# Kernel tuning notes

Hardware: AMD Instinct MI355X
Metric: run time of the kernel (lower is better)

The kernel has to match this reference:

```python
import jax, jax.numpy as jnp
import numpy as np

HEAD_DIM = 128
NUM_Q_HEADS = 16
NUM_KV_HEADS = 8
EPS = 1e-6


def _rope_tables(seq_len, head_dim, base=10000.0):
    inv_freq = 1.0 / (base ** (np.arange(0, head_dim, 2, dtype=np.float32) / head_dim))
    t = np.arange(seq_len, dtype=np.float32)
    freqs = np.outer(t, inv_freq)                      # [S, hd/2]
    emb = np.concatenate([freqs, freqs], axis=-1)      # [S, hd]
    return jnp.asarray(np.cos(emb)), jnp.asarray(np.sin(emb))


def setup_inputs() -> dict:
    key = jax.random.key(0)
    k1, k2, k3 = jax.random.split(key, 3)
    B, S, D = 2, 2048, 2048
    qo_dim = NUM_Q_HEADS * HEAD_DIM
    kv_dim = NUM_KV_HEADS * HEAD_DIM
    x = jax.random.normal(k1, (B, S, D), dtype=jnp.float32)
    w_qkv = jax.random.normal(k2, (qo_dim + 2 * kv_dim, D), dtype=jnp.float32) * 0.02
    w_o = jax.random.normal(k3, (D, qo_dim), dtype=jnp.float32) * 0.02
    pos_cos, pos_sin = _rope_tables(S, HEAD_DIM)
    return {
        "x": x,
        "pos_cos": pos_cos,
        "pos_sin": pos_sin,
        "w_qkv": w_qkv,
        "w_o": w_o,
        "q_norm_w": jnp.ones((HEAD_DIM,), dtype=jnp.float32),
        "k_norm_w": jnp.ones((HEAD_DIM,), dtype=jnp.float32),
    }


def _rms_norm(h, w):
    # per-head RMSNorm over last dim (head_dim)
    var = jnp.mean(jnp.square(h), axis=-1, keepdims=True)
    return h * jax.lax.rsqrt(var + EPS) * w


def _rotate_half(h):
    h1, h2 = jnp.split(h, 2, axis=-1)
    return jnp.concatenate([-h2, h1], axis=-1)


def _apply_rope(h, cos, sin):
    # h: [B, S, H, hd]; cos/sin: [S, hd]
    c = cos[None, :, None, :]
    s = sin[None, :, None, :]
    return h * c + _rotate_half(h) * s


def reference(x, pos_cos, pos_sin, w_qkv, w_o, q_norm_w, k_norm_w):
    B, S, D = x.shape
    hd = HEAD_DIM
    qkv = jnp.einsum("bsd,ed->bse", x, w_qkv).reshape(B, S, -1, hd)
    q = qkv[:, :, :NUM_Q_HEADS]                                   # [B,S,Hq,hd]
    k = qkv[:, :, NUM_Q_HEADS:NUM_Q_HEADS + NUM_KV_HEADS]         # [B,S,Hk,hd]
    v = qkv[:, :, NUM_Q_HEADS + NUM_KV_HEADS:]                    # [B,S,Hk,hd]

    q = _apply_rope(_rms_norm(q, q_norm_w), pos_cos, pos_sin)
    k = _apply_rope(_rms_norm(k, k_norm_w), pos_cos, pos_sin)

    # GQA: expand kv heads to match query heads
    rep = NUM_Q_HEADS // NUM_KV_HEADS
    k = jnp.repeat(k, rep, axis=2)
    v = jnp.repeat(v, rep, axis=2)

    scale = 1.0 / jnp.sqrt(jnp.float32(hd))
    scores = jnp.einsum("bqhd,bkhd->bhqk", q, k) * scale          # [B,H,S,S]
    causal = jnp.tril(jnp.ones((S, S), dtype=bool))
    scores = jnp.where(causal[None, None], scores, jnp.finfo(scores.dtype).min)
    attn = jax.nn.softmax(scores, axis=-1)
    out = jnp.einsum("bhqk,bkhd->bqhd", attn, v)                  # [B,S,H,hd]
    out = out.reshape(B, S, NUM_Q_HEADS * hd)
    return jnp.einsum("bse,de->bsd", out, w_o)
```

## Files before the change

### kernel.cpp

```cpp
#include <hip/hip_runtime.h>
#include <hip/hip_bf16.h>
#include <stdint.h>

#define HD 128
#define NQH 16
#define NKVH 8
#define SEQ 2048
#define DMODEL 2048
#define BATCH 2

typedef __attribute__((ext_vector_type(8))) short bf16x8;
typedef __attribute__((ext_vector_type(4))) float f32x4;
typedef __attribute__((ext_vector_type(16))) float f32x16;

__device__ __forceinline__ ushort f2bf(float f){
  union { float f; uint32_t u; } v; v.f = f;
  uint32_t u = v.u;
  return (ushort)((u + 0x7FFFu + ((u >> 16) & 1u)) >> 16);
}
__device__ __forceinline__ float bf2f(ushort h){
  union { uint32_t u; float f; } v; v.u = ((uint32_t)h) << 16; return v.f;
}
__device__ __forceinline__ void gload16(const void* g, void* l){
  __builtin_amdgcn_global_load_lds((const __attribute__((address_space(1))) void*)g,
                                   (__attribute__((address_space(3))) void*)l, 16, 0, 0);
}
__device__ __forceinline__ unsigned int cvtpk(float lo, float hi){
  unsigned int r;
  asm("v_cvt_pk_bf16_f32 %0, %1, %2" : "=v"(r) : "v"(lo), "v"(hi));
  return r;
}

__global__ void cvtbf3(const float* __restrict__ x, const float* __restrict__ wqkv,
                       const float* __restrict__ wo,
                       ushort* __restrict__ xb, ushort* __restrict__ wqkvb,
                       ushort* __restrict__ wob){
  int bid = blockIdx.x;
  const float* in; ushort* out; int i;
  if (bid < 8192)       { in = x;    out = xb;    i = bid*256 + threadIdx.x; }
  else if (bid < 16384) { in = wqkv; out = wqkvb; i = (bid-8192)*256 + threadIdx.x; }
  else                  { in = wo;   out = wob;   i = (bid-16384)*256 + threadIdx.x; }
  float4 v = ((const float4*)in)[i];
  ushort4 o;
  o.x = f2bf(v.x); o.y = f2bf(v.y); o.z = f2bf(v.z); o.w = f2bf(v.w);
  ((ushort4*)out)[i] = o;
}

template<int OUTF32>
__global__ __launch_bounds__(256) void gemm_bt(const ushort* __restrict__ A,
                                               const ushort* __restrict__ B,
                                               void* __restrict__ C,
                                               int M, int N, int K){
  __shared__ __align__(16) ushort lA[128*64];
  __shared__ __align__(16) ushort lB[128*64];
  const int tid = threadIdx.x;
  const int l = tid & 63, w = tid >> 6;
  const int nwg = gridDim.x * gridDim.y;
  const int lin = blockIdx.y * gridDim.x + blockIdx.x;
  const int wg = (lin & 7) * (nwg >> 3) + (lin >> 3);
  const int m0 = (wg / gridDim.x) * 128, n0 = (wg % gridDim.x) * 128;
  const int wr = (w >> 1) * 64, wc = (w & 1) * 64;
  f32x4 acc[4][4];
  #pragma unroll
  for (int m=0;m<4;m++)
    #pragma unroll
    for (int n=0;n<4;n++) acc[m][n] = f32x4{0.f,0.f,0.f,0.f};

  const int srow = l >> 3;
  const int scol = ((l & 7) ^ srow) << 3;
  const ushort* gA = A + (size_t)(m0 + w*32 + srow) * K + scol;
  const ushort* gB = B + (size_t)(n0 + w*32 + srow) * K + scol;
  ushort* lAw = &lA[(w*32) * 64];
  ushort* lBw = &lB[(w*32) * 64];

  for (int kt = 0; kt < K; kt += 64){
    __syncthreads();
    #pragma unroll
    for (int j=0;j<4;j++){
      gload16(gA + kt + (size_t)(j*8)*K, lAw + j*8*64);
      gload16(gB + kt + (size_t)(j*8)*K, lBw + j*8*64);
    }
    __syncthreads();
    #pragma unroll
    for (int kk=0; kk<2; kk++){
      bf16x8 af[4], bb[4];
      #pragma unroll
      for (int m=0;m<4;m++){
        int row = wr + m*16 + (l & 15);
        int slot = (kk*4 + (l >> 4)) ^ (row & 7);
        af[m] = *(const bf16x8*)&lA[row*64 + slot*8];
      }
      #pragma unroll
      for (int n=0;n<4;n++){
        int row = wc + n*16 + (l & 15);
        int slot = (kk*4 + (l >> 4)) ^ (row & 7);
        bb[n] = *(const bf16x8*)&lB[row*64 + slot*8];
      }
      #pragma unroll
      for (int m=0;m<4;m++)
        #pragma unroll
        for (int n=0;n<4;n++)
          acc[m][n] = __builtin_amdgcn_mfma_f32_16x16x32_bf16(af[m], bb[n], acc[m][n], 0,0,0);
    }
  }
  #pragma unroll
  for (int m=0;m<4;m++)
    #pragma unroll
    for (int n=0;n<4;n++)
      #pragma unroll
      for (int r=0;r<4;r++){
        size_t row = (size_t)(m0 + wr + m*16 + (l>>4)*4 + r);
        size_t col = (size_t)(n0 + wc + n*16 + (l & 15));
        float v = acc[m][n][r];
        if (OUTF32) ((float*)C)[row*N + col] = v;
        else        ((ushort*)C)[row*N + col] = f2bf(v);
      }
}

__global__ __launch_bounds__(512, 1) void gemm256_bt(const ushort* __restrict__ A,
                                                     const ushort* __restrict__ B,
                                                     ushort* __restrict__ C,
                                                     int M, int N, int K){
  __shared__ __align__(16) ushort lA[2][256*64];
  __shared__ __align__(16) ushort lB[2][256*64];
  const int tid = threadIdx.x;
  const int l = tid & 63, w = tid >> 6;
  const int wm = w >> 2, wn = w & 3;
  const int nwg = gridDim.x * gridDim.y;
  const int lin = blockIdx.y * gridDim.x + blockIdx.x;
  const int wg = (lin & 7) * (nwg >> 3) + (lin >> 3);
  const int m0 = (wg / gridDim.x) * 256, n0 = (wg % gridDim.x) * 256;
  const int NT = K >> 6;

  const int srow = w*8 + (l >> 3);
  const int scol = ((l & 7) ^ (l >> 3)) << 3;

  const int la15 = l & 15;
  const int sl0 = (((l >> 4)    ) ^ (l & 7)) * 8;
  const int sl1 = ((4 + (l >> 4)) ^ (l & 7)) * 8;

  f32x4 acc[8][4];
  #pragma unroll
  for (int m=0;m<8;m++)
    #pragma unroll
    for (int n=0;n<4;n++) acc[m][n] = f32x4{0.f,0.f,0.f,0.f};

  auto stgA = [&](int t, int h){
    const int bi = t & 1;
    #pragma unroll
    for (int j=0;j<2;j++)
      gload16(A + (size_t)(m0 + h*128 + j*64 + srow)*K + t*64 + scol,
              &lA[bi][(h*128 + j*64 + w*8)*64]);
  };
  auto stgB = [&](int t, int h){
    const int bi = t & 1;
    #pragma unroll
    for (int j=0;j<2;j++)
      gload16(B + (size_t)(n0 + h*128 + j*64 + srow)*K + t*64 + scol,
              &lB[bi][(h*128 + j*64 + w*8)*64]);
  };

  stgA(0,0); stgA(0,1); stgB(0,0); stgB(0,1);
  stgA(1,0); stgB(1,0); stgB(1,1);
  asm volatile("s_waitcnt vmcnt(6)" ::: "memory");
  __builtin_amdgcn_s_barrier();

  for (int t2=0; t2<NT; t2+=2){
    #pragma unroll
    for (int tt=0; tt<2; tt++){
      const int t = t2 + tt;
      const ushort* pA = &lA[tt][(wm*128 + la15)*64];
      const ushort* pB = &lB[tt][(wn*64  + la15)*64];
      bf16x8 bfr0[4], bfr1[4];
      #pragma unroll
      for (int q=0; q<4; q++){
        bf16x8 af0[2], af1[2];
        #pragma unroll
        for (int mi2=0; mi2<2; mi2++){
          af0[mi2] = *(const bf16x8*)(pA + (q*32 + mi2*16)*64 + sl0);
          af1[mi2] = *(const bf16x8*)(pA + (q*32 + mi2*16)*64 + sl1);
        }
        if (q == 0){
          #pragma unroll
          for (int ni=0; ni<4; ni++){
            bfr0[ni] = *(const bf16x8*)(pB + ni*16*64 + sl0);
            bfr1[ni] = *(const bf16x8*)(pB + ni*16*64 + sl1);
          }
        }
        if (q == 0 && t+1 < NT) stgA(t+1, 1);
        if (q == 1 && t+2 < NT) stgB(t+2, 0);
        if (q == 2 && t+2 < NT) stgB(t+2, 1);
        __builtin_amdgcn_s_barrier();
        asm volatile("s_waitcnt lgkmcnt(0)" ::: "memory");
        if (q == 3 && t+2 < NT) stgA(t+2, 0);
        __builtin_amdgcn_s_setprio(1);
        #pragma unroll
        for (int mi2=0; mi2<2; mi2++)
          #pragma unroll
          for (int ni=0; ni<4; ni++)
            acc[q*2+mi2][ni] = __builtin_amdgcn_mfma_f32_16x16x32_bf16(
                af0[mi2], bfr0[ni], acc[q*2+mi2][ni], 0,0,0);
        #pragma unroll
        for (int mi2=0; mi2<2; mi2++)
          #pragma unroll
          for (int ni=0; ni<4; ni++)
            acc[q*2+mi2][ni] = __builtin_amdgcn_mfma_f32_16x16x32_bf16(
                af1[mi2], bfr1[ni], acc[q*2+mi2][ni], 0,0,0);
        __builtin_amdgcn_s_setprio(0);
        if (q == 3){
          if (t < NT-2) { asm volatile("s_waitcnt vmcnt(6)" ::: "memory"); }
          else          { asm volatile("s_waitcnt vmcnt(0)" ::: "memory"); }
        }
        __builtin_amdgcn_s_barrier();
      }
    }
  }

  #pragma unroll
  for (int mi=0; mi<8; mi++)
    #pragma unroll
    for (int ni=0; ni<4; ni++)
      #pragma unroll
      for (int r=0; r<4; r++){
        size_t row = (size_t)(m0 + wm*128 + mi*16 + (l>>4)*4 + r);
        size_t col = (size_t)(n0 + wn*64 + ni*16 + (l & 15));
        C[row*N + col] = f2bf(acc[mi][ni][r]);
      }
}

__global__ __launch_bounds__(256) void nr_vt(const ushort* __restrict__ qkv,
                                             const float* __restrict__ cosT,
                                             const float* __restrict__ sinT,
                                             const float* __restrict__ qw,
                                             const float* __restrict__ kw,
                                             ushort* __restrict__ Qo,
                                             ushort* __restrict__ Ko,
                                             ushort* __restrict__ vt){
  if (blockIdx.x < 24576){
    int gw = (blockIdx.x * 256 + threadIdx.x) >> 6;
    int l = threadIdx.x & 63;
    int head = gw % 24;
    int bs = gw / 24;
    int s = bs & (SEQ-1);
    int b = bs >> 11;
    ushort2 hv = *(const ushort2*)(qkv + (size_t)bs*(2*DMODEL) + head*HD + l*2);
    float h0 = bf2f(hv.x), h1 = bf2f(hv.y);
    float ss = h0*h0 + h1*h1;
    #pragma unroll
    for (int m=1; m<64; m<<=1) ss += __shfl_xor(ss, m);
    float rinv = rsqrtf(ss * (1.0f/128.0f) + 1e-6f);
    const float* wp = (head < NQH) ? qw : kw;
    float w0 = wp[l*2], w1 = wp[l*2+1];
    float n0 = h0 * rinv * w0, n1 = h1 * rinv * w1;
    float p0 = __shfl_xor(n0, 32), p1 = __shfl_xor(n1, 32);
    float r0 = (l < 32) ? -p0 : p0;
    float r1 = (l < 32) ? -p1 : p1;
    float c0 = cosT[s*HD + l*2], c1 = cosT[s*HD + l*2 + 1];
    float s0 = sinT[s*HD + l*2], s1 = sinT[s*HD + l*2 + 1];
    float sc = (head < NQH) ? 0.12751656062f : 1.0f;
    ushort2 o;
    o.x = f2bf((n0*c0 + r0*s0) * sc);
    o.y = f2bf((n1*c1 + r1*s1) * sc);
    if (head < NQH)
      *(ushort2*)(Qo + ((size_t)((b*NQH + head)*SEQ) + s)*HD + l*2) = o;
    else
      *(ushort2*)(Ko + ((size_t)((b*NKVH + (head-NQH))*SEQ) + s)*HD + l*2) = o;
  } else {
    __shared__ __align__(16) ushort t[64][136];
    int bid = blockIdx.x - 24576;
    int st = bid & 31, kh = (bid >> 5) & 7, b = bid >> 8;
    int s0 = st * 64;
    int tid = threadIdx.x;
    #pragma unroll
    for (int it=0; it<4; it++){
      int row = (tid >> 4) + it*16;
      int c = tid & 15;
      uint4 v = *(const uint4*)&qkv[((size_t)(b*SEQ + s0 + row))*(2*DMODEL) + (NQH+NKVH+kh)*HD + c*8];
      *(uint4*)&t[row][c*8] = v;
    }
    __syncthreads();
    #pragma unroll
    for (int it=0; it<4; it++){
      int g = it*256 + tid;
      int d = g >> 3, c = g & 7;
      ushort tmp[8] __attribute__((aligned(16)));
      #pragma unroll
      for (int j=0;j<8;j++) tmp[j] = t[c*8+j][d];
      *(uint4*)&vt[((size_t)((b*NKVH+kh)*HD + d))*SEQ + s0 + c*8] = *(uint4*)tmp;
    }
  }
}

__global__ __launch_bounds__(256, 2) void attn_fwd(const ushort* __restrict__ Q,
                                                   const ushort* __restrict__ Kb,
                                                   const ushort* __restrict__ Vt,
                                                   ushort* __restrict__ O){
  __shared__ __align__(16) ushort lK[2][64*128];
  __shared__ __align__(16) ushort lV[2][128*64];
  const int l = threadIdx.x & 63, w = threadIdx.x >> 6;
  const int wq = w >> 1, wkv = w & 1;
  const int hl = l >> 5, q32 = l & 31;
  const int lin = blockIdx.x;
  const int wg = (lin & 7) * 64 + (lin >> 3);
  const int e = wg & 15, head = (wg >> 4) & 15, b = wg >> 8;
  const int kh = head >> 1;

  const ushort* kg = Kb + (size_t)((b*NKVH + kh)*SEQ) * HD;
  const ushort* vg = Vt + (size_t)((b*NKVH + kh)*HD) * SEQ;

  auto STAGE = [&](int t, int bi){
    const int kv0 = t*64;
    #pragma unroll
    for (int j=0;j<4;j++){
      int krow = kv0 + w*16 + j*4 + (l>>4);
      gload16(kg + (size_t)krow*HD + (((l&15) ^ (krow&15))<<3),
              &lK[bi][(w*16 + j*4)*128]);
      int vrow = w*32 + j*8 + (l>>3);
      gload16(vg + (size_t)vrow*SEQ + kv0 + (((l&7) ^ (l>>3))<<3),
              &lV[bi][(w*32 + j*8)*64]);
    }
  };

  auto run_tile = [&](int qt){
    const int qb = qt*64 + wq*32;
    const ushort* qp = Q + ((size_t)((b*NQH + head)*SEQ) + qb + q32) * HD + hl*8;
    bf16x8 qf[8];
    #pragma unroll
    for (int ks=0; ks<8; ks++) qf[ks] = *(const bf16x8*)(qp + ks*16);

    float mrun = -1e30f, lrun = 0.f;
    f32x16 acc[4];
    #pragma unroll
    for (int dt=0;dt<4;dt++)
      #pragma unroll
      for (int r=0;r<16;r++) acc[dt][r] = 0.f;

    STAGE(0, 0);

    for (int t=0; t<=qt; t++){
      const int bi = t & 1;
      if (t < qt){
        STAGE(t+1, bi^1);
        asm volatile("s_waitcnt vmcnt(8)" ::: "memory");
      } else {
        asm volatile("s_waitcnt vmcnt(0)" ::: "memory");
      }
      __builtin_amdgcn_s_barrier();

      const bool skip = (t==qt) && (wq==0) && (wkv==1);
      if (!skip){
        f32x16 sa, sb;
        #pragma unroll
        for (int r=0;r<16;r++){ sa[r] = 0.f; sb[r] = 0.f; }
        const int rowT = wkv*32 + q32;
        __builtin_amdgcn_s_setprio(1);
        #pragma unroll
        for (int ks=0; ks<4; ks++){
          int slot0 = (ks*2 + hl) ^ (rowT & 15);
          int slot1 = ((ks+4)*2 + hl) ^ (rowT & 15);
          bf16x8 kf0 = *(const bf16x8*)&lK[bi][rowT*128 + slot0*8];
          bf16x8 kf1 = *(const bf16x8*)&lK[bi][rowT*128 + slot1*8];
          sa = __builtin_amdgcn_mfma_f32_32x32x16_bf16(kf0, qf[ks],   sa, 0,0,0);
          sb = __builtin_amdgcn_mfma_f32_32x32x16_bf16(kf1, qf[ks+4], sb, 0,0,0);
        }
        __builtin_amdgcn_s_setprio(0);
        f32x16 s = sa + sb;
        if (t==qt && wq==wkv){
          const int qg = qb + q32;
          #pragma unroll
          for (int r=0;r<16;r++){
            int kvg = t*64 + wkv*32 + (r&3) + 8*(r>>2) + 4*hl;
            s[r] = (kvg > qg) ? -1e30f : s[r];
          }
        }
        float m0 = fmaxf(fmaxf(s[0],s[1]),s[2]);
        float m1 = fmaxf(fmaxf(s[3],s[4]),s[5]);
        float m2 = fmaxf(fmaxf(s[6],s[7]),s[8]);
        float m3 = fmaxf(fmaxf(s[9],s[10]),s[11]);
        float m4 = fmaxf(fmaxf(s[12],s[13]),s[14]);
        float tmax = fmaxf(fmaxf(fmaxf(m0,m1),fmaxf(m2,m3)),fmaxf(m4,s[15]));
        tmax = fmaxf(tmax, __shfl_xor(tmax, 32));
        if (!__all(tmax <= mrun + 8.f)){
          float mnew = fmaxf(mrun, tmax);
          float corr = __builtin_amdgcn_exp2f(mrun - mnew);
          mrun = mnew; lrun *= corr;
          #pragma unroll
          for (int r=0;r<16;r++){
            int qr = (r&3) + 8*(r>>2) + 4*hl;
            float cr = __shfl(corr, qr);
            acc[0][r]*=cr; acc[1][r]*=cr; acc[2][r]*=cr; acc[3][r]*=cr;
          }
        }
        #pragma unroll
        for (int r=0;r<16;r++) s[r] = __builtin_amdgcn_exp2f(s[r] - mrun);
        float r0s = (s[0]+s[1])+(s[2]+s[3]);
        float r1s = (s[4]+s[5])+(s[6]+s[7]);
        float r2s = (s[8]+s[9])+(s[10]+s[11]);
        float r3s = (s[12]+s[13])+(s[14]+s[15]);
        float rs = (r0s+r1s)+(r2s+r3s);
        rs += __shfl_xor(rs, 32);
        lrun += rs;
        union PWU { unsigned int u[4]; bf16x8 v; };
        PWU pw0, pw1;
        {
          unsigned int A = cvtpk(s[0], s[1]);
          unsigned int B = cvtpk(s[2], s[3]);
          unsigned int C = cvtpk(s[4], s[5]);
          unsigned int D = cvtpk(s[6], s[7]);
          auto sw0 = __builtin_amdgcn_permlane32_swap(A, C, false, false);
          auto sw1 = __builtin_amdgcn_permlane32_swap(B, D, false, false);
          pw0.u[0]=sw0[0]; pw0.u[1]=sw1[0]; pw0.u[2]=sw0[1]; pw0.u[3]=sw1[1];
        }
        {
          unsigned int A = cvtpk(s[8], s[9]);
          unsigned int B = cvtpk(s[10], s[11]);
          unsigned int C = cvtpk(s[12], s[13]);
          unsigned int D = cvtpk(s[14], s[15]);
          auto sw0 = __builtin_amdgcn_permlane32_swap(A, C, false, false);
          auto sw1 = __builtin_amdgcn_permlane32_swap(B, D, false, false);
          pw1.u[0]=sw0[0]; pw1.u[1]=sw1[0]; pw1.u[2]=sw0[1]; pw1.u[3]=sw1[1];
        }
        __builtin_amdgcn_s_setprio(1);
        #pragma unroll
        for (int dt=0; dt<4; dt++){
          int d = dt*32 + q32;
          int slot0 = (wkv*4 + 0 + hl) ^ (d & 7);
          bf16x8 vf0 = *(const bf16x8*)&lV[bi][d*64 + slot0*8];
          acc[dt] = __builtin_amdgcn_mfma_f32_32x32x16_bf16(pw0.v, vf0, acc[dt], 0,0,0);
        }
        #pragma unroll
        for (int dt=0; dt<4; dt++){
          int d = dt*32 + q32;
          int slot1 = (wkv*4 + 2 + hl) ^ (d & 7);
          bf16x8 vf1 = *(const bf16x8*)&lV[bi][d*64 + slot1*8];
          acc[dt] = __builtin_amdgcn_mfma_f32_32x32x16_bf16(pw1.v, vf1, acc[dt], 0,0,0);
        }
        __builtin_amdgcn_s_setprio(0);
      }
      asm volatile("s_waitcnt lgkmcnt(0)" ::: "memory");
      __builtin_amdgcn_s_barrier();
    }

    float* mergeO = (float*)(&lK[0][0]) + wq*4096;
    float* mergeML = (float*)(&lV[0][0]);
    if (wkv == 1){
      #pragma unroll
      for (int dt=0; dt<4; dt++)
        #pragma unroll
        for (int rg=0; rg<4; rg++){
          f32x4 o = { acc[dt][rg*4+0], acc[dt][rg*4+1], acc[dt][rg*4+2], acc[dt][rg*4+3] };
          *(f32x4*)&mergeO[(dt*4+rg)*256 + l*4] = o;
        }
      if (l < 32){
        mergeML[wq*64 + l] = mrun;
        mergeML[wq*64 + 32 + l] = lrun;
      }
    }
    __syncthreads();
    if (wkv == 0){
      float m1 = mergeML[wq*64 + q32];
      float l1 = mergeML[wq*64 + 32 + q32];
      float mf = fmaxf(mrun, m1);
      float c0 = __builtin_amdgcn_exp2f(mrun - mf);
      float c1 = __builtin_amdgcn_exp2f(m1 - mf);
      float lt = lrun*c0 + l1*c1;
      float linv = 1.0f / lt;
      float f0 = c0 * linv, f1 = c1 * linv;
      float g0a[16], g1a[16];
      #pragma unroll
      for (int r=0;r<16;r++){
        int qr = (r&3) + 8*(r>>2) + 4*hl;
        g0a[r] = __shfl(f0, qr);
        g1a[r] = __shfl(f1, qr);
      }
      #pragma unroll
      for (int dt=0; dt<4; dt++)
        #pragma unroll
        for (int rg=0; rg<4; rg++){
          f32x4 o1 = *(const f32x4*)&mergeO[(dt*4+rg)*256 + l*4];
          #pragma unroll
          for (int j=0;j<4;j++){
            int r = rg*4 + j;
            int qr = (r&3) + 8*(r>>2) + 4*hl;
            float val = acc[dt][r]*g0a[r] + o1[j]*g1a[r];
            int orow = qt*64 + wq*32 + qr;
            O[((size_t)(b*SEQ) + orow)*DMODEL + head*HD + dt*32 + q32] = f2bf(val);
          }
        }
    }
    __syncthreads();
  };

  run_tile(e);
  run_tile(31 - e);
}

extern "C" void kernel_launch(void* const* d_in, const int* in_sizes, int n_in,
                              void* d_out, int out_size, void* d_ws, size_t ws_size,
                              hipStream_t stream){
  const float* x    = (const float*)d_in[0];
  const float* pcos = (const float*)d_in[1];
  const float* psin = (const float*)d_in[2];
  const float* wqkv = (const float*)d_in[3];
  const float* wo   = (const float*)d_in[4];
  const float* qnw  = (const float*)d_in[5];
  const float* knw  = (const float*)d_in[6];
  char* ws = (char*)d_ws;

  ushort* xb    = (ushort*)(ws + 0);
  ushort* wqkvb = (ushort*)(ws + 16777216);
  ushort* wob   = (ushort*)(ws + 33554432);
  ushort* qkv   = (ushort*)(ws + 41943040);
  ushort* qbuf  = (ushort*)(ws + 75497472);
  ushort* kbuf  = (ushort*)(ws + 92274688);
  ushort* vtb   = (ushort*)(ws + 100663296);
  ushort* aout  = (ushort*)(ws + 0);

  cvtbf3<<<20480, 256, 0, stream>>>(x, wqkv, wo, xb, wqkvb, wob);

  gemm256_bt<<<dim3(16,16), 512, 0, stream>>>(xb, wqkvb, qkv, 4096, 4096, 2048);

  nr_vt<<<25088, 256, 0, stream>>>(qkv, pcos, psin, qnw, knw, qbuf, kbuf, vtb);

  attn_fwd<<<dim3(512), 256, 0, stream>>>(qbuf, kbuf, vtb, aout);

  gemm_bt<1><<<dim3(16,32), 256, 0, stream>>>(aout, wob, d_out, 4096, 2048, 2048);
}
```

Measured before the change: 198.7 us.

## Double-buffer LDS fragment reads in GEMM to overlap with MFMA

Restructures the gemm256_bt inner loop so the A/B register fragments for the next quarter-step (and the next K tile) are read from LDS right after the current MFMAs issue, using ping-pong register buffers. This removes one barrier per sub-step and hides LDS read latency behind matrix math. In exchange it needs more VGPRs for the duplicated fragment buffers, and the reordered barriers and waits must still keep LDS reads from racing with the async global-to-LDS loads.

```diff
diff --git a/kernel.cpp b/kernel.cpp
--- a/kernel.cpp
+++ b/kernel.cpp
@@ -117,6 +117,21 @@
       }
 }
 
+#define RDA(TT, Q, DST) { const ushort* pA_ = &lA[TT][(wm*128 + la15)*64]; \
+  DST[0] = *(const bf16x8*)(pA_ + ((Q)*32 +  0)*64 + sl0); \
+  DST[1] = *(const bf16x8*)(pA_ + ((Q)*32 +  0)*64 + sl1); \
+  DST[2] = *(const bf16x8*)(pA_ + ((Q)*32 + 16)*64 + sl0); \
+  DST[3] = *(const bf16x8*)(pA_ + ((Q)*32 + 16)*64 + sl1); }
+#define RDB(TT, DST) { const ushort* pB_ = &lB[TT][(wn*64 + la15)*64]; \
+  DST[0] = *(const bf16x8*)(pB_ +  0*64 + sl0); \
+  DST[1] = *(const bf16x8*)(pB_ +  0*64 + sl1); \
+  DST[2] = *(const bf16x8*)(pB_ + 16*64 + sl0); \
+  DST[3] = *(const bf16x8*)(pB_ + 16*64 + sl1); \
+  DST[4] = *(const bf16x8*)(pB_ + 32*64 + sl0); \
+  DST[5] = *(const bf16x8*)(pB_ + 32*64 + sl1); \
+  DST[6] = *(const bf16x8*)(pB_ + 48*64 + sl0); \
+  DST[7] = *(const bf16x8*)(pB_ + 48*64 + sl1); }
+
 __global__ __launch_bounds__(512, 1) void gemm256_bt(const ushort* __restrict__ A,
                                                      const ushort* __restrict__ B,
                                                      ushort* __restrict__ C,
@@ -160,38 +175,27 @@
               &lB[bi][(h*128 + j*64 + w*8)*64]);
   };
 
+  bf16x8 afb[2][4];
+  bf16x8 bfb[2][8];
+
   stgA(0,0); stgA(0,1); stgB(0,0); stgB(0,1);
   stgA(1,0); stgB(1,0); stgB(1,1);
   asm volatile("s_waitcnt vmcnt(6)" ::: "memory");
+  RDA(0, 0, afb[0]);
+  RDB(0, bfb[0]);
   __builtin_amdgcn_s_barrier();
 
   for (int t2=0; t2<NT; t2+=2){
     #pragma unroll
     for (int tt=0; tt<2; tt++){
       const int t = t2 + tt;
-      const ushort* pA = &lA[tt][(wm*128 + la15)*64];
-      const ushort* pB = &lB[tt][(wn*64  + la15)*64];
-      bf16x8 bfr0[4], bfr1[4];
       #pragma unroll
       for (int q=0; q<4; q++){
-        bf16x8 af0[2], af1[2];
-        #pragma unroll
-        for (int mi2=0; mi2<2; mi2++){
-          af0[mi2] = *(const bf16x8*)(pA + (q*32 + mi2*16)*64 + sl0);
-          af1[mi2] = *(const bf16x8*)(pA + (q*32 + mi2*16)*64 + sl1);
-        }
-        if (q == 0){
-          #pragma unroll
-          for (int ni=0; ni<4; ni++){
-            bfr0[ni] = *(const bf16x8*)(pB + ni*16*64 + sl0);
-            bfr1[ni] = *(const bf16x8*)(pB + ni*16*64 + sl1);
-          }
-        }
+        const int cur = q & 1, nxt = cur ^ 1;
+        asm volatile("s_waitcnt lgkmcnt(0)" ::: "memory");
         if (q == 0 && t+1 < NT) stgA(t+1, 1);
         if (q == 1 && t+2 < NT) stgB(t+2, 0);
         if (q == 2 && t+2 < NT) stgB(t+2, 1);
-        __builtin_amdgcn_s_barrier();
-        asm volatile("s_waitcnt lgkmcnt(0)" ::: "memory");
         if (q == 3 && t+2 < NT) stgA(t+2, 0);
         __builtin_amdgcn_s_setprio(1);
         #pragma unroll
@@ -199,17 +203,23 @@
           #pragma unroll
           for (int ni=0; ni<4; ni++)
             acc[q*2+mi2][ni] = __builtin_amdgcn_mfma_f32_16x16x32_bf16(
-                af0[mi2], bfr0[ni], acc[q*2+mi2][ni], 0,0,0);
+                afb[cur][mi2*2+0], bfb[tt][ni*2+0], acc[q*2+mi2][ni], 0,0,0);
         #pragma unroll
         for (int mi2=0; mi2<2; mi2++)
           #pragma unroll
           for (int ni=0; ni<4; ni++)
             acc[q*2+mi2][ni] = __builtin_amdgcn_mfma_f32_16x16x32_bf16(
-                af1[mi2], bfr1[ni], acc[q*2+mi2][ni], 0,0,0);
+                afb[cur][mi2*2+1], bfb[tt][ni*2+1], acc[q*2+mi2][ni], 0,0,0);
         __builtin_amdgcn_s_setprio(0);
-        if (q == 3){
+        if (q < 3){
+          RDA(tt, q+1, afb[nxt]);
+        } else {
           if (t < NT-2) { asm volatile("s_waitcnt vmcnt(6)" ::: "memory"); }
           else          { asm volatile("s_waitcnt vmcnt(0)" ::: "memory"); }
+          if (t+1 < NT){
+            RDA(tt^1, 0, afb[nxt]);
+            RDB(tt^1, bfb[tt^1]);
+          }
         }
         __builtin_amdgcn_s_barrier();
       }
```

Measured after the change: 261.0 us. 31.3% more time.
